# Kernel optimization log

Hardware: AMD Instinct MI355X
Metric: run time of the kernel (lower is better)

## Reference

```python
import jax, jax.numpy as jnp
import numpy as np

B, T, U = 4, 256, 100
H_ENC, H_DEC = 512, 512
INPUT_SIZE = H_ENC + H_DEC  # 1024, joint='concat'
INNER = 512
VOCAB = 1024


def setup_inputs() -> dict:
    key = jax.random.key(0)
    k1, k2, k3, k4, k5, k6 = jax.random.split(key, 6)
    s_in = 1.0 / np.sqrt(INPUT_SIZE)
    s_h = 1.0 / np.sqrt(INNER)
    return {
        "enc_state": jax.random.normal(k1, (B, T, H_ENC), dtype=jnp.float32),
        "dec_state": jax.random.normal(k2, (B, U, H_DEC), dtype=jnp.float32),
        # mlp[0]: Linear(input_size -> inner): W1 [inner, input_size], b1 [inner]
        "W1": jax.random.uniform(k3, (INNER, INPUT_SIZE), jnp.float32, -s_in, s_in),
        "b1": jax.random.uniform(k4, (INNER,), jnp.float32, -s_in, s_in),
        # mlp[2]: Linear(inner -> vocab): W2 [vocab, inner], b2 [vocab]
        "W2": jax.random.uniform(k5, (VOCAB, INNER), jnp.float32, -s_h, s_h),
        "b2": jax.random.uniform(k6, (VOCAB,), jnp.float32, -s_h, s_h),
    }


def reference(enc_state, dec_state, W1, b1, W2, b2):
    # joint='concat': concat([enc broadcast over U, dec broadcast over T], -1)
    # then Linear -> tanh -> Linear.
    # Mathematically identical fused form: split W1 into enc/dec column blocks,
    # project each at native size, broadcast-add.
    h_enc = H_ENC
    W1e = W1[:, :h_enc]   # [inner, H_enc]
    W1d = W1[:, h_enc:]   # [inner, H_dec]
    pe = jnp.einsum('bth,ih->bti', enc_state, W1e)  # [B,T,inner]
    pd = jnp.einsum('buh,ih->bui', dec_state, W1d)  # [B,U,inner]
    hidden = jnp.tanh(pe[:, :, None, :] + pd[:, None, :, :] + b1)  # [B,T,U,inner]
    joint = jnp.einsum('btui,vi->btuv', hidden, W2) + b2  # [B,T,U,vocab]
    return joint
```

## Files before the change

kernel.cpp:

```cpp
#include <hip/hip_runtime.h>
#include <hip/hip_bf16.h>

#define NB 4
#define NT 256
#define NU 100
#define NH 512
#define NI 512
#define NV 1024
#define MROWS (NB * NT * NU)

typedef __attribute__((ext_vector_type(4))) float f32x4;
typedef __attribute__((ext_vector_type(8))) __bf16 bf16x8;

static __device__ __forceinline__ unsigned int f2bf(float f) {
  unsigned int u = __float_as_uint(f);
  return (u + 0x7FFFu + ((u >> 16) & 1u)) >> 16;
}

static __device__ __forceinline__ float fast_tanh(float x) {
  float e = __expf(2.f * x);
  return 1.f - 2.f * __builtin_amdgcn_rcpf(1.f + e);
}

static __device__ __forceinline__ unsigned int cvt_pk_bf16(float lo, float hi) {
  unsigned int r;
  asm("v_cvt_pk_bf16_f32 %0, %1, %2" : "=v"(r) : "v"(lo), "v"(hi));
  return r;
}

__global__ __launch_bounds__(256) void proj_kernel(
    const float* __restrict__ enc, const float* __restrict__ dec,
    const float* __restrict__ W1, float* __restrict__ pe, float* __restrict__ pd) {
  __shared__ float As[64][17];
  __shared__ float Bs[64][17];
  const int bx = blockIdx.x;
  const float* A;
  float* P;
  int Mrows, colOff, row0;
  if (bx < 16) { A = enc; P = pe; Mrows = NB * NT; colOff = 0;  row0 = bx * 64; }
  else         { A = dec; P = pd; Mrows = NB * NU; colOff = NH; row0 = (bx - 16) * 64; }
  const int col0 = blockIdx.y * 64;
  const int tx = threadIdx.x;
  const int tr = tx >> 4, tc = tx & 15;
  const int lr = tx >> 2, lc = (tx & 3) * 4;
  float acc[4][4] = {};
  for (int k0 = 0; k0 < NH; k0 += 16) {
    float4 av = make_float4(0.f, 0.f, 0.f, 0.f);
    if (row0 + lr < Mrows)
      av = *(const float4*)(A + (size_t)(row0 + lr) * NH + k0 + lc);
    float4 bv = *(const float4*)(W1 + (size_t)(col0 + lr) * (NH + NH) + colOff + k0 + lc);
    As[lr][lc] = av.x; As[lr][lc + 1] = av.y; As[lr][lc + 2] = av.z; As[lr][lc + 3] = av.w;
    Bs[lr][lc] = bv.x; Bs[lr][lc + 1] = bv.y; Bs[lr][lc + 2] = bv.z; Bs[lr][lc + 3] = bv.w;
    __syncthreads();
#pragma unroll
    for (int kk = 0; kk < 16; ++kk) {
      float a4[4], b4[4];
#pragma unroll
      for (int i = 0; i < 4; ++i) { a4[i] = As[tr * 4 + i][kk]; b4[i] = Bs[tc * 4 + i][kk]; }
#pragma unroll
      for (int i = 0; i < 4; ++i)
#pragma unroll
        for (int j = 0; j < 4; ++j) acc[i][j] = fmaf(a4[i], b4[j], acc[i][j]);
    }
    __syncthreads();
  }
#pragma unroll
  for (int i = 0; i < 4; ++i) {
    int r = row0 + tr * 4 + i;
    if (r < Mrows) {
#pragma unroll
      for (int j = 0; j < 4; ++j)
        P[(size_t)r * NI + col0 + tc * 4 + j] = acc[i][j];
    }
  }
}

__global__ __launch_bounds__(256) void cvt_w2_frag_kernel(
    const float* __restrict__ W2, unsigned short* __restrict__ w2f) {
  int g = blockIdx.x * 256 + threadIdx.x;
  int lr = g & 15, lq = (g >> 4) & 3;
  int cb = (g >> 6) & 15, kt = (g >> 10) & 15, nt = (g >> 14) & 3;
  int v = nt * 256 + cb * 16 + lr;
  int k = kt * 32 + lq * 8;
  const float* src = W2 + (size_t)v * NI + k;
  float4 a = *(const float4*)src;
  float4 b = *(const float4*)(src + 4);
  uint4 o;
  o.x = f2bf(a.x) | (f2bf(a.y) << 16);
  o.y = f2bf(a.z) | (f2bf(a.w) << 16);
  o.z = f2bf(b.x) | (f2bf(b.y) << 16);
  o.w = f2bf(b.z) | (f2bf(b.w) << 16);
  *(uint4*)(w2f + (size_t)g * 8) = o;
}

__global__ __launch_bounds__(512, 4) void fused_joint_kernel(
    const float* __restrict__ pe, const float* __restrict__ pd,
    const float* __restrict__ b1, const unsigned short* __restrict__ w2f,
    const float* __restrict__ b2, float* __restrict__ out) {
  __shared__ unsigned char ldsA[65536];
  const int tx = threadIdx.x;
  const int R0 = blockIdx.x * 64;
  const int lane = tx & 63, wid = tx >> 6;
  const int wr = wid >> 2, wc = wid & 3;
  const int lr = lane & 15, lq = lane >> 4;

  const unsigned short* w2base = w2f + ((size_t)(wc * 4) * 64 + lq * 16 + lr) * 8;
#define LOADB(DST, G) do {                                                    \
    const unsigned short* s_ = w2base + ((size_t)(G) << 13);                  \
    DST##0 = *(const bf16x8*)(s_);                                            \
    DST##1 = *(const bf16x8*)(s_ + 512);                                      \
    DST##2 = *(const bf16x8*)(s_ + 1024);                                     \
    DST##3 = *(const bf16x8*)(s_ + 1536);                                     \
  } while (0)

  bf16x8 bA0, bA1, bA2, bA3, bB0, bB1, bB2, bB3;
  LOADB(bA, 0);

#pragma unroll 2
  for (int pass = 0; pass < 8; ++pass) {
    int idx = pass * 512 + tx;
    int row = idx >> 6;
    int g8 = idx & 63;
    int i0 = g8 * 8;
    int grow = R0 + row;
    int b = grow / (NT * NU);
    int rem = grow - b * (NT * NU);
    int t = rem / NU;
    int u = rem - t * NU;
    const float* peP = pe + (size_t)(b * NT + t) * NI + i0;
    const float* pdP = pd + (size_t)(b * NU + u) * NI + i0;
    float4 p0 = *(const float4*)peP, p1 = *(const float4*)(peP + 4);
    float4 q0 = *(const float4*)pdP, q1 = *(const float4*)(pdP + 4);
    float4 c0 = *(const float4*)(b1 + i0), c1 = *(const float4*)(b1 + i0 + 4);
    uint4 pk;
    pk.x = cvt_pk_bf16(fast_tanh(p0.x + q0.x + c0.x), fast_tanh(p0.y + q0.y + c0.y));
    pk.y = cvt_pk_bf16(fast_tanh(p0.z + q0.z + c0.z), fast_tanh(p0.w + q0.w + c0.w));
    pk.z = cvt_pk_bf16(fast_tanh(p1.x + q1.x + c1.x), fast_tanh(p1.y + q1.y + c1.y));
    pk.w = cvt_pk_bf16(fast_tanh(p1.z + q1.z + c1.z), fast_tanh(p1.w + q1.w + c1.w));
    *(uint4*)(ldsA + row * 1024 + ((g8 ^ (row & 7)) << 4)) = pk;
  }
  __syncthreads();

  f32x4 acc[2][4];
#pragma unroll
  for (int mf = 0; mf < 2; ++mf)
#pragma unroll
    for (int nf = 0; nf < 4; ++nf)
#pragma unroll
      for (int z = 0; z < 4; ++z) acc[mf][nf][z] = 0.f;

#define COMPUTE(BV, G) do {                                                   \
    const int kt_ = (G) & 15;                                                 \
    bf16x8 af_[2];                                                            \
    _Pragma("unroll")                                                         \
    for (int mf = 0; mf < 2; ++mf) {                                          \
      int row_ = wr * 32 + mf * 16 + lr;                                      \
      af_[mf] = *(const bf16x8*)(ldsA + row_ * 1024 +                         \
                                 (((kt_ * 4 + lq) ^ (lr & 7)) << 4));         \
    }                                                                         \
    __builtin_amdgcn_s_setprio(1);                                            \
    _Pragma("unroll")                                                         \
    for (int mf = 0; mf < 2; ++mf) {                                          \
      acc[mf][0] = __builtin_amdgcn_mfma_f32_16x16x32_bf16(af_[mf], BV##0, acc[mf][0], 0, 0, 0); \
      acc[mf][1] = __builtin_amdgcn_mfma_f32_16x16x32_bf16(af_[mf], BV##1, acc[mf][1], 0, 0, 0); \
      acc[mf][2] = __builtin_amdgcn_mfma_f32_16x16x32_bf16(af_[mf], BV##2, acc[mf][2], 0, 0, 0); \
      acc[mf][3] = __builtin_amdgcn_mfma_f32_16x16x32_bf16(af_[mf], BV##3, acc[mf][3], 0, 0, 0); \
    }                                                                         \
    __builtin_amdgcn_s_setprio(0);                                            \
    if (kt_ == 15) {                                                          \
      const int np_ = (G) >> 4;                                               \
      _Pragma("unroll")                                                       \
      for (int nf = 0; nf < 4; ++nf) {                                        \
        int col_ = np_ * 256 + wc * 64 + nf * 16 + lr;                        \
        float bb_ = b2[col_];                                                 \
        _Pragma("unroll")                                                     \
        for (int mf = 0; mf < 2; ++mf) {                                      \
          _Pragma("unroll")                                                   \
          for (int j = 0; j < 4; ++j) {                                       \
            int grow_ = R0 + wr * 32 + mf * 16 + lq * 4 + j;                  \
            out[(size_t)grow_ * NV + col_] = acc[mf][nf][j] + bb_;            \
            acc[mf][nf][j] = 0.f;                                             \
          }                                                                   \
        }                                                                     \
      }                                                                       \
    }                                                                         \
  } while (0)

  for (int g = 0; g < 64; g += 2) {
    LOADB(bB, g + 1);
    COMPUTE(bA, g);
    if (g + 2 < 64) LOADB(bA, g + 2);
    COMPUTE(bB, g + 1);
  }
#undef COMPUTE
#undef LOADB
}

extern "C" void kernel_launch(void* const* d_in, const int* in_sizes, int n_in,
                              void* d_out, int out_size, void* d_ws, size_t ws_size,
                              hipStream_t stream) {
  const float* enc = (const float*)d_in[0];
  const float* dec = (const float*)d_in[1];
  const float* W1  = (const float*)d_in[2];
  const float* b1  = (const float*)d_in[3];
  const float* W2  = (const float*)d_in[4];
  const float* b2  = (const float*)d_in[5];
  float* out = (float*)d_out;
  char* ws = (char*)d_ws;

  float* pe = (float*)ws;
  float* pd = (float*)(ws + (2u << 20));
  unsigned short* w2f = (unsigned short*)(ws + (3u << 20));

  proj_kernel<<<dim3(23, 8), 256, 0, stream>>>(enc, dec, W1, pe, pd);
  cvt_w2_frag_kernel<<<256, 256, 0, stream>>>(W2, w2f);
  fused_joint_kernel<<<MROWS / 64, 512, 0, stream>>>(pe, pd, b1, w2f, b2, out);
}
```

Baseline: 227.5 us.

## Switch joint GEMM to 32x32x16 MFMA with deeper B prefetch, merge prep kernels

Replaces the 16x16x32 bf16 MFMA tiles in the fused joint kernel with 32x32x16 MFMA, so each wave issues fewer, larger instructions and makes fewer LDS A-fragment reads. W2 is repacked into a matching fragment layout, and B fragments are prefetched four steps ahead instead of one. The W2 conversion is folded into the projection kernel as extra blocks, which removes one launch. In exchange, accumulator registers now form two 16-wide vectors, and the output store pattern changes to 32-column rows, which may change coalescing and register pressure.

```diff
diff --git a/kernel.cpp b/kernel.cpp
--- a/kernel.cpp
+++ b/kernel.cpp
@@ -9,7 +9,7 @@
 #define NV 1024
 #define MROWS (NB * NT * NU)
 
-typedef __attribute__((ext_vector_type(4))) float f32x4;
+typedef __attribute__((ext_vector_type(16))) float f32x16;
 typedef __attribute__((ext_vector_type(8))) __bf16 bf16x8;
 
 static __device__ __forceinline__ unsigned int f2bf(float f) {
@@ -28,19 +28,37 @@
   return r;
 }
 
-__global__ __launch_bounds__(256) void proj_kernel(
+__global__ __launch_bounds__(256) void prep_kernel(
     const float* __restrict__ enc, const float* __restrict__ dec,
-    const float* __restrict__ W1, float* __restrict__ pe, float* __restrict__ pd) {
+    const float* __restrict__ W1, const float* __restrict__ W2,
+    float* __restrict__ pe, float* __restrict__ pd,
+    unsigned short* __restrict__ w2g) {
+  const int bx = blockIdx.x;
+  const int tx = threadIdx.x;
+  if (bx >= 23) {
+    int c = ((bx - 23) * 8 + blockIdx.y) * 256 + tx;
+    int lane = c & 63, ntl = (c >> 6) & 7, ks = (c >> 9) & 31, np = c >> 14;
+    int col = np * 256 + ntl * 32 + (lane & 31);
+    int k = ks * 16 + (lane >> 5) * 8;
+    const float* src = W2 + (size_t)col * NI + k;
+    float4 a = *(const float4*)src;
+    float4 b = *(const float4*)(src + 4);
+    uint4 o;
+    o.x = f2bf(a.x) | (f2bf(a.y) << 16);
+    o.y = f2bf(a.z) | (f2bf(a.w) << 16);
+    o.z = f2bf(b.x) | (f2bf(b.y) << 16);
+    o.w = f2bf(b.z) | (f2bf(b.w) << 16);
+    *(uint4*)(w2g + (size_t)c * 8) = o;
+    return;
+  }
   __shared__ float As[64][17];
   __shared__ float Bs[64][17];
-  const int bx = blockIdx.x;
   const float* A;
   float* P;
   int Mrows, colOff, row0;
   if (bx < 16) { A = enc; P = pe; Mrows = NB * NT; colOff = 0;  row0 = bx * 64; }
   else         { A = dec; P = pd; Mrows = NB * NU; colOff = NH; row0 = (bx - 16) * 64; }
   const int col0 = blockIdx.y * 64;
-  const int tx = threadIdx.x;
   const int tr = tx >> 4, tc = tx & 15;
   const int lr = tx >> 2, lc = (tx & 3) * 4;
   float acc[4][4] = {};
@@ -75,46 +93,28 @@
   }
 }
 
-__global__ __launch_bounds__(256) void cvt_w2_frag_kernel(
-    const float* __restrict__ W2, unsigned short* __restrict__ w2f) {
-  int g = blockIdx.x * 256 + threadIdx.x;
-  int lr = g & 15, lq = (g >> 4) & 3;
-  int cb = (g >> 6) & 15, kt = (g >> 10) & 15, nt = (g >> 14) & 3;
-  int v = nt * 256 + cb * 16 + lr;
-  int k = kt * 32 + lq * 8;
-  const float* src = W2 + (size_t)v * NI + k;
-  float4 a = *(const float4*)src;
-  float4 b = *(const float4*)(src + 4);
-  uint4 o;
-  o.x = f2bf(a.x) | (f2bf(a.y) << 16);
-  o.y = f2bf(a.z) | (f2bf(a.w) << 16);
-  o.z = f2bf(b.x) | (f2bf(b.y) << 16);
-  o.w = f2bf(b.z) | (f2bf(b.w) << 16);
-  *(uint4*)(w2f + (size_t)g * 8) = o;
-}
-
 __global__ __launch_bounds__(512, 4) void fused_joint_kernel(
     const float* __restrict__ pe, const float* __restrict__ pd,
-    const float* __restrict__ b1, const unsigned short* __restrict__ w2f,
+    const float* __restrict__ b1, const unsigned short* __restrict__ w2g,
     const float* __restrict__ b2, float* __restrict__ out) {
   __shared__ unsigned char ldsA[65536];
   const int tx = threadIdx.x;
   const int R0 = blockIdx.x * 64;
   const int lane = tx & 63, wid = tx >> 6;
   const int wr = wid >> 2, wc = wid & 3;
-  const int lr = lane & 15, lq = lane >> 4;
-
-  const unsigned short* w2base = w2f + ((size_t)(wc * 4) * 64 + lq * 16 + lr) * 8;
-#define LOADB(DST, G) do {                                                    \
-    const unsigned short* s_ = w2base + ((size_t)(G) << 13);                  \
-    DST##0 = *(const bf16x8*)(s_);                                            \
-    DST##1 = *(const bf16x8*)(s_ + 512);                                      \
-    DST##2 = *(const bf16x8*)(s_ + 1024);                                     \
-    DST##3 = *(const bf16x8*)(s_ + 1536);                                     \
+  const int l31 = lane & 31, lh = lane >> 5;
+
+  const unsigned char* w2p = (const unsigned char*)w2g;
+  const unsigned char* bBase0 = w2p + ((wc * 2 + 0) * 64 + lane) * 16;
+  const unsigned char* bBase1 = w2p + ((wc * 2 + 1) * 64 + lane) * 16;
+
+#define LOADB(SET, G) do {                                                    \
+    SET##0 = *(const bf16x8*)(bBase0 + ((size_t)(G) << 13));                  \
+    SET##1 = *(const bf16x8*)(bBase1 + ((size_t)(G) << 13));                  \
   } while (0)
 
-  bf16x8 bA0, bA1, bA2, bA3, bB0, bB1, bB2, bB3;
-  LOADB(bA, 0);
+  bf16x8 s00, s01, s10, s11, s20, s21, s30, s31;
+  LOADB(s0, 0); LOADB(s1, 1); LOADB(s2, 2); LOADB(s3, 3);
 
 #pragma unroll 2
   for (int pass = 0; pass < 8; ++pass) {
@@ -141,58 +141,45 @@
   }
   __syncthreads();
 
-  f32x4 acc[2][4];
-#pragma unroll
-  for (int mf = 0; mf < 2; ++mf)
-#pragma unroll
-    for (int nf = 0; nf < 4; ++nf)
-#pragma unroll
-      for (int z = 0; z < 4; ++z) acc[mf][nf][z] = 0.f;
-
-#define COMPUTE(BV, G) do {                                                   \
-    const int kt_ = (G) & 15;                                                 \
-    bf16x8 af_[2];                                                            \
-    _Pragma("unroll")                                                         \
-    for (int mf = 0; mf < 2; ++mf) {                                          \
-      int row_ = wr * 32 + mf * 16 + lr;                                      \
-      af_[mf] = *(const bf16x8*)(ldsA + row_ * 1024 +                         \
-                                 (((kt_ * 4 + lq) ^ (lr & 7)) << 4));         \
-    }                                                                         \
+  f32x16 acc0, acc1;
+#pragma unroll
+  for (int z = 0; z < 16; ++z) { acc0[z] = 0.f; acc1[z] = 0.f; }
+
+  const int aRowBase = (wr * 32 + l31) * 1024;
+  const int rx = l31 & 7;
+
+#define STEP(SET, G) do {                                                     \
+    const int ks_ = (G) & 31;                                                 \
+    bf16x8 af_ = *(const bf16x8*)(ldsA + aRowBase +                           \
+                                  (((ks_ * 2 + lh) ^ rx) << 4));              \
     __builtin_amdgcn_s_setprio(1);                                            \
-    _Pragma("unroll")                                                         \
-    for (int mf = 0; mf < 2; ++mf) {                                          \
-      acc[mf][0] = __builtin_amdgcn_mfma_f32_16x16x32_bf16(af_[mf], BV##0, acc[mf][0], 0, 0, 0); \
-      acc[mf][1] = __builtin_amdgcn_mfma_f32_16x16x32_bf16(af_[mf], BV##1, acc[mf][1], 0, 0, 0); \
-      acc[mf][2] = __builtin_amdgcn_mfma_f32_16x16x32_bf16(af_[mf], BV##2, acc[mf][2], 0, 0, 0); \
-      acc[mf][3] = __builtin_amdgcn_mfma_f32_16x16x32_bf16(af_[mf], BV##3, acc[mf][3], 0, 0, 0); \
-    }                                                                         \
+    acc0 = __builtin_amdgcn_mfma_f32_32x32x16_bf16(af_, SET##0, acc0, 0, 0, 0); \
+    acc1 = __builtin_amdgcn_mfma_f32_32x32x16_bf16(af_, SET##1, acc1, 0, 0, 0); \
     __builtin_amdgcn_s_setprio(0);                                            \
-    if (kt_ == 15) {                                                          \
-      const int np_ = (G) >> 4;                                               \
+    if (ks_ == 31) {                                                          \
+      const int np_ = (G) >> 5;                                               \
+      int c0_ = np_ * 256 + wc * 64 + l31;                                    \
+      float bb0_ = b2[c0_];                                                   \
+      float bb1_ = b2[c0_ + 32];                                              \
       _Pragma("unroll")                                                       \
-      for (int nf = 0; nf < 4; ++nf) {                                        \
-        int col_ = np_ * 256 + wc * 64 + nf * 16 + lr;                        \
-        float bb_ = b2[col_];                                                 \
-        _Pragma("unroll")                                                     \
-        for (int mf = 0; mf < 2; ++mf) {                                      \
-          _Pragma("unroll")                                                   \
-          for (int j = 0; j < 4; ++j) {                                       \
-            int grow_ = R0 + wr * 32 + mf * 16 + lq * 4 + j;                  \
-            out[(size_t)grow_ * NV + col_] = acc[mf][nf][j] + bb_;            \
-            acc[mf][nf][j] = 0.f;                                             \
-          }                                                                   \
-        }                                                                     \
+      for (int r_ = 0; r_ < 16; ++r_) {                                       \
+        int grow_ = R0 + wr * 32 + (r_ & 3) + 8 * (r_ >> 2) + 4 * lh;         \
+        float* op_ = out + (size_t)grow_ * NV + c0_;                          \
+        op_[0]  = acc0[r_] + bb0_;                                            \
+        op_[32] = acc1[r_] + bb1_;                                            \
+        acc0[r_] = 0.f;                                                       \
+        acc1[r_] = 0.f;                                                       \
       }                                                                       \
     }                                                                         \
   } while (0)
 
-  for (int g = 0; g < 64; g += 2) {
-    LOADB(bB, g + 1);
-    COMPUTE(bA, g);
-    if (g + 2 < 64) LOADB(bA, g + 2);
-    COMPUTE(bB, g + 1);
-  }
-#undef COMPUTE
+  for (int g = 0; g < 128; g += 4) {
+    STEP(s0, g);     if (g + 4 < 128) LOADB(s0, g + 4);
+    STEP(s1, g + 1); if (g + 5 < 128) LOADB(s1, g + 5);
+    STEP(s2, g + 2); if (g + 6 < 128) LOADB(s2, g + 6);
+    STEP(s3, g + 3); if (g + 7 < 128) LOADB(s3, g + 7);
+  }
+#undef STEP
 #undef LOADB
 }
 
@@ -210,9 +197,8 @@
 
   float* pe = (float*)ws;
   float* pd = (float*)(ws + (2u << 20));
-  unsigned short* w2f = (unsigned short*)(ws + (3u << 20));
-
-  proj_kernel<<<dim3(23, 8), 256, 0, stream>>>(enc, dec, W1, pe, pd);
-  cvt_w2_frag_kernel<<<256, 256, 0, stream>>>(W2, w2f);
-  fused_joint_kernel<<<MROWS / 64, 512, 0, stream>>>(pe, pd, b1, w2f, b2, out);
-}
+  unsigned short* w2g = (unsigned short*)(ws + (3u << 20));
+
+  prep_kernel<<<dim3(55, 8), 256, 0, stream>>>(enc, dec, W1, W2, pe, pd, w2g);
+  fused_joint_kernel<<<MROWS / 64, 512, 0, stream>>>(pe, pd, b1, w2g, b2, out);
+}
```

Result: slower. 259.0 us (+13.8%).
